# Performance work log

Hardware: AMD Instinct MI355X
Metric: run time of the kernel (lower is better)

The kernel has to match this reference:

```python
import jax, jax.numpy as jnp
import numpy as np

S, N, C = 256, 512, 32   # n_seq, n_res, channels
EPS = 1e-3               # module eps for mask normalization
LN_EPS = 1e-5            # torch LayerNorm default eps


def setup_inputs() -> dict:
    key = jax.random.key(0)
    ks = jax.random.split(key, 6)
    scale = 1.0 / np.sqrt(C)
    return {
        "m": jax.random.normal(ks[0], (S, N, C), jnp.float32),
        "mask": jnp.ones((S, N), jnp.float32),
        "ln_gamma": jnp.ones((C,), jnp.float32),
        "ln_beta": jnp.zeros((C,), jnp.float32),
        "Wa": jax.random.normal(ks[1], (C, C), jnp.float32) * scale,
        "ba": jnp.zeros((C,), jnp.float32),
        "Wb": jax.random.normal(ks[2], (C, C), jnp.float32) * scale,
        "bb": jnp.zeros((C,), jnp.float32),
        "Wout": jax.random.normal(ks[3], (C * C, C), jnp.float32) * (1.0 / np.sqrt(C * C)),
        "bout": jnp.zeros((C,), jnp.float32),
    }


def reference(m, mask, ln_gamma, ln_beta, Wa, ba, Wb, bb, Wout, bout):
    # LayerNorm over channel dim
    mu = jnp.mean(m, axis=-1, keepdims=True)
    var = jnp.mean(jnp.square(m - mu), axis=-1, keepdims=True)
    mh = (m - mu) * jax.lax.rsqrt(var + LN_EPS) * ln_gamma + ln_beta  # [S, N, C]

    # dual linear projections, masked per (seq, res), then seq<->res transpose
    a = jnp.swapaxes((mh @ Wa + ba) * mask[..., None], -2, -3)  # [N, S, C]
    b = jnp.swapaxes((mh @ Wb + bb) * mask[..., None], -2, -3)  # [N, S, C]

    # outer product summed over sequences: [N, N, C, C] -> [N, N, C*C]
    outer = jnp.einsum("bac,dae->bdce", a, b).reshape(N, N, C * C)
    outer = outer @ Wout + bout  # [N, N, C]

    # pairwise mask normalization: sum over seqs of mask[s,i]*mask[s,j]
    norm = jnp.einsum("ab,ad->bd", mask, mask)[..., None] + EPS  # [N, N, 1]
    return outer / norm
```

## Files before the change

### kernel.cpp

```cpp
#include <hip/hip_runtime.h>

#define S_SEQ 256
#define N_RES 512
#define CCH   32

typedef __attribute__((ext_vector_type(8))) short bf16x8;
typedef __attribute__((ext_vector_type(4))) float f32x4;
typedef __attribute__((ext_vector_type(2))) unsigned int u32x2;

__device__ __forceinline__ unsigned short f2bf(float x) {
    unsigned int u = __float_as_uint(x);
    return (unsigned short)((u + 0x7FFFu + ((u >> 16) & 1u)) >> 16);
}

#define GLOAD_LDS16(gp, lp) __builtin_amdgcn_global_load_lds( \
    (const __attribute__((address_space(1))) unsigned int*)(gp), \
    (__attribute__((address_space(3))) unsigned int*)(lp), 16, 0, 0)

#define BAR()    do { __builtin_amdgcn_s_barrier(); asm volatile("" ::: "memory"); } while (0)
#define WLGKM0() asm volatile("s_waitcnt lgkmcnt(0)" ::: "memory")
#define WVM(n)   asm volatile("s_waitcnt vmcnt(" #n ")" ::: "memory")

__global__ __launch_bounds__(256) void prep_ab(
    const float* __restrict__ m, const float* __restrict__ mask,
    const float* __restrict__ gam, const float* __restrict__ bet,
    const float* __restrict__ Wa, const float* __restrict__ ba,
    const float* __restrict__ Wb, const float* __restrict__ bb,
    char* __restrict__ Ag, char* __restrict__ Bg)
{
    __shared__ float WaL[1024], WbL[1024];
    __shared__ float gL[32], btL[32], baL[32], bbL[32];
    __shared__ unsigned short At[32 * 256];
    __shared__ unsigned short Bt[32 * 256];

    const int n = blockIdx.x;
    const int t = threadIdx.x;

    for (int i = t; i < 1024; i += 256) { WaL[i] = Wa[i]; WbL[i] = Wb[i]; }
    if (t < 32) { gL[t] = gam[t]; btL[t] = bet[t]; baL[t] = ba[t]; bbL[t] = bb[t]; }
    __syncthreads();

    const int s = t;
    float mv[32];
    const float* mrow = m + ((size_t)s * N_RES + n) * CCH;
#pragma unroll
    for (int c4 = 0; c4 < 8; c4++) {
        f32x4 v = *(const f32x4*)(mrow + c4 * 4);
        mv[c4 * 4 + 0] = v.x; mv[c4 * 4 + 1] = v.y;
        mv[c4 * 4 + 2] = v.z; mv[c4 * 4 + 3] = v.w;
    }
    float mu = 0.f;
#pragma unroll
    for (int c = 0; c < 32; c++) mu += mv[c];
    mu *= (1.f / 32.f);
    float var = 0.f;
#pragma unroll
    for (int c = 0; c < 32; c++) { float d = mv[c] - mu; var += d * d; }
    var *= (1.f / 32.f);
    float rs = rsqrtf(var + 1e-5f);
    float mh[32];
#pragma unroll
    for (int c = 0; c < 32; c++) mh[c] = (mv[c] - mu) * rs * gL[c] + btL[c];

    const float msk = mask[(size_t)s * N_RES + n];

    f32x4 av[8], bv[8];
#pragma unroll
    for (int cg = 0; cg < 8; cg++) { av[cg] = (f32x4)0.f; bv[cg] = (f32x4)0.f; }
#pragma unroll
    for (int k = 0; k < 32; k++) {
        float x = mh[k];
#pragma unroll
        for (int cg = 0; cg < 8; cg++) {
            f32x4 wa4 = *(const f32x4*)&WaL[k * 32 + cg * 4];
            f32x4 wb4 = *(const f32x4*)&WbL[k * 32 + cg * 4];
            av[cg] += x * wa4;
            bv[cg] += x * wb4;
        }
    }
#pragma unroll
    for (int cg = 0; cg < 8; cg++) {
#pragma unroll
        for (int u = 0; u < 4; u++) {
            int c = cg * 4 + u;
            At[c * 256 + s] = f2bf((av[cg][u] + baL[c]) * msk);
            Bt[c * 256 + s] = f2bf((bv[cg][u] + bbL[c]) * msk);
        }
    }
    __syncthreads();

    const size_t tbase = (size_t)(n >> 2) * 65536;
    const int halfq = ((n >> 1) & 1) << 2;
    const int irb = (n & 1) * 32;
#pragma unroll
    for (int u = 0; u < 4; u++) {
        int cid = t * 4 + u;
        int c = cid >> 5, g = cid & 31;
        int kt = g >> 2, q = g & 3;
        size_t off = tbase + (size_t)kt * 8192 + (size_t)(irb + c) * 128
                   + (size_t)(((halfq | q) ^ (c & 7)) << 4);
        *(uint4*)(Ag + off) = *(const uint4*)(At + c * 256 + g * 8);
        *(uint4*)(Bg + off) = *(const uint4*)(Bt + c * 256 + g * 8);
    }
}

__global__ __launch_bounds__(256) void kwt(const float* __restrict__ Wout,
                                           unsigned short* __restrict__ Wt3)
{
    int idx = blockIdx.x * 256 + threadIdx.x;
    int e = idx >> 10, ch = (idx >> 5) & 31, c = idx & 31;
    Wt3[idx] = f2bf(Wout[(size_t)(c * 32 + e) * 32 + ch]);
}

__global__ __launch_bounds__(256) void knorm(const float* __restrict__ mask,
                                             float* __restrict__ inv_norm)
{
    __shared__ float Mi[64][65];
    __shared__ float Mj[64][65];
    const int bi = blockIdx.x >> 3, bj = blockIdx.x & 7;
    const int t = threadIdx.x;
    const int ty = t >> 4, tx = t & 15;

    float acc[4][4];
#pragma unroll
    for (int a = 0; a < 4; a++)
#pragma unroll
        for (int b = 0; b < 4; b++) acc[a][b] = 0.f;

    for (int sc = 0; sc < 4; sc++) {
        for (int e = t; e < 4096; e += 256) {
            int sr = e >> 6, col = e & 63;
            Mi[sr][col] = mask[(size_t)(sc * 64 + sr) * N_RES + bi * 64 + col];
            Mj[sr][col] = mask[(size_t)(sc * 64 + sr) * N_RES + bj * 64 + col];
        }
        __syncthreads();
        for (int sp = 0; sp < 64; sp++) {
#pragma unroll
            for (int a = 0; a < 4; a++)
#pragma unroll
                for (int b = 0; b < 4; b++)
                    acc[a][b] += Mi[sp][ty * 4 + a] * Mj[sp][tx * 4 + b];
        }
        __syncthreads();
    }
#pragma unroll
    for (int a = 0; a < 4; a++)
#pragma unroll
        for (int b = 0; b < 4; b++) {
            int i = bi * 64 + ty * 4 + a;
            int j = bj * 64 + tx * 4 + b;
            inv_norm[(size_t)i * N_RES + j] = 1.f / (acc[a][b] + 1e-3f);
        }
}

__global__ __launch_bounds__(256, 4) void kmain9(
    const char* __restrict__ Ag, const char* __restrict__ Bg,
    const unsigned short* __restrict__ Wt3, const float* __restrict__ inv_norm,
    const float* __restrict__ bout, float* __restrict__ out)
{
    __shared__ __align__(16) char sm[33024];

    const int bid = blockIdx.x;
    const int xcd = bid & 7;
    const int xidx = bid >> 3;
    const int TI = xcd * 16 + ((xidx >> 5) & 15);
    const int TJ = (xidx >> 9) * 32 + (xidx & 31);

    const int t = threadIdx.x;
    const int lane = t & 63, wid = t >> 6;
    const int wr = wid >> 1, wc = wid & 1;
    const int rl = lane & 15, h4 = lane >> 4;

    const char* pa = Ag + (size_t)TI * 65536;
    const char* pb = Bg + (size_t)TJ * 65536;

#define SH(kt) do { \
    char* db_ = sm + (((kt) & 1) * 16384); \
    GLOAD_LDS16(pa + (kt) * 8192 + t * 16,        db_ + t * 16); \
    GLOAD_LDS16(pa + (kt) * 8192 + 4096 + t * 16, db_ + 4096 + t * 16); \
    GLOAD_LDS16(pb + (kt) * 8192 + t * 16,        db_ + 8192 + t * 16); \
    GLOAD_LDS16(pb + (kt) * 8192 + 4096 + t * 16, db_ + 12288 + t * 16); \
} while (0)

    const int abase = rl * 128 + (((((wr << 2) | h4)) ^ (rl & 7)) << 4);
    const int bbase = 8192 + rl * 128 + (((((wc << 2) | h4)) ^ (rl & 7)) << 4);

    f32x4 acc[4][4];
#pragma unroll
    for (int a = 0; a < 4; a++)
#pragma unroll
        for (int b = 0; b < 4; b++) acc[a][b] = (f32x4)0.f;

    SH(0);
    SH(1);

#pragma unroll
    for (int kt = 0; kt < 8; kt++) {
        if (kt < 7) { WVM(4); } else { WVM(0); }
        BAR();
        const char* buf = sm + ((kt & 1) * 16384);
        bf16x8 af[4], bfr[4];
#pragma unroll
        for (int am = 0; am < 4; am++)
            af[am] = *(const bf16x8*)(buf + abase + am * 2048);
#pragma unroll
        for (int bn = 0; bn < 4; bn++)
            bfr[bn] = *(const bf16x8*)(buf + bbase + bn * 2048);
        __builtin_amdgcn_s_setprio(1);
#pragma unroll
        for (int am = 0; am < 4; am++)
#pragma unroll
            for (int bn = 0; bn < 4; bn++)
                acc[am][bn] = __builtin_amdgcn_mfma_f32_16x16x32_bf16(
                    af[am], bfr[bn], acc[am][bn], 0, 0, 0);
        __builtin_amdgcn_s_setprio(0);
        BAR();
        if (kt <= 5) SH(kt + 2);
    }
#undef SH

#pragma unroll
    for (int am = 0; am < 4; am++) {
        const int cs = ((am & 1) << 1) + (h4 >> 1);
#pragma unroll
        for (int bn = 0; bn < 4; bn++) {
            const int p = (wr * 2 + (am >> 1)) * 4 + wc * 2 + (bn >> 1);
            const int e = ((bn & 1) << 4) + rl;
            unsigned int lo = (unsigned int)f2bf(acc[am][bn][0]) |
                              ((unsigned int)f2bf(acc[am][bn][1]) << 16);
            unsigned int hi = (unsigned int)f2bf(acc[am][bn][2]) |
                              ((unsigned int)f2bf(acc[am][bn][3]) << 16);
            u32x2 wv; wv[0] = lo; wv[1] = hi;
            *(u32x2*)(sm + p * 2064 + e * 64 +
                      ((cs ^ ((e >> 1) & 3)) << 4) + ((h4 & 1) << 3)) = wv;
        }
    }
    WLGKM0();
    BAR();

    const int kq = wid;
    f32x4 ae0 = (f32x4)0.f, ae1 = (f32x4)0.f;
    const char* grow = sm + rl * 2064;
#pragma unroll
    for (int es = 0; es < 8; es++) {
        const int e = kq * 8 + es;
        bf16x8 ga = *(const bf16x8*)(grow + e * 64 + ((h4 ^ ((e >> 1) & 3)) << 4));
        bf16x8 wb0 = *(const bf16x8*)(Wt3 + (size_t)e * 1024 + rl * 32 + h4 * 8);
        bf16x8 wb1 = *(const bf16x8*)(Wt3 + (size_t)e * 1024 + (16 + rl) * 32 + h4 * 8);
        ae0 = __builtin_amdgcn_mfma_f32_16x16x32_bf16(ga, wb0, ae0, 0, 0, 0);
        ae1 = __builtin_amdgcn_mfma_f32_16x16x32_bf16(ga, wb1, ae1, 0, 0, 0);
    }
    BAR();

    float* ps = (float*)sm;
#pragma unroll
    for (int r = 0; r < 4; r++) {
        ps[(kq * 16 + h4 * 4 + r) * 34 + rl]      = ae0[r];
        ps[(kq * 16 + h4 * 4 + r) * 34 + 16 + rl] = ae1[r];
    }
    WLGKM0();
    BAR();

#pragma unroll
    for (int u = 0; u < 2; u++) {
        const int idx = u * 256 + t;
        const int p = idx >> 5, ch = idx & 31;
        float v = 0.f;
#pragma unroll
        for (int k2 = 0; k2 < 4; k2++)
            v += ps[(k2 * 16 + p) * 34 + ch];
        const int i = TI * 4 + (p >> 2), j = TJ * 4 + (p & 3);
        out[((size_t)(i * N_RES + j)) * CCH + ch] =
            (v + bout[ch]) * inv_norm[(size_t)i * N_RES + j];
    }
}

extern "C" void kernel_launch(void* const* d_in, const int* in_sizes, int n_in,
                              void* d_out, int out_size, void* d_ws, size_t ws_size,
                              hipStream_t stream)
{
    const float* m    = (const float*)d_in[0];
    const float* mask = (const float*)d_in[1];
    const float* gam  = (const float*)d_in[2];
    const float* bet  = (const float*)d_in[3];
    const float* Wa   = (const float*)d_in[4];
    const float* ba   = (const float*)d_in[5];
    const float* Wb   = (const float*)d_in[6];
    const float* bb   = (const float*)d_in[7];
    const float* Wout = (const float*)d_in[8];
    const float* bout = (const float*)d_in[9];
    float* out = (float*)d_out;

    char* ws = (char*)d_ws;
    char* Ag = ws;
    char* Bg = ws + 8388608;
    unsigned short* Wt3 = (unsigned short*)(ws + 16777216);
    float* inv_norm = (float*)(ws + 16842752);

    prep_ab<<<dim3(N_RES), dim3(256), 0, stream>>>(m, mask, gam, bet, Wa, ba, Wb, bb, Ag, Bg);
    kwt<<<dim3(128), dim3(256), 0, stream>>>(Wout, Wt3);
    knorm<<<dim3(64), dim3(256), 0, stream>>>(mask, inv_norm);
    kmain9<<<dim3(16384), dim3(256), 0, stream>>>(Ag, Bg, Wt3, inv_norm, bout, out);
}
```

Baseline: 202.0 us.

## Load A operand directly from global into registers, stage only B in LDS

The prep kernel now writes A in a plain row-major layout, so the main kernel can load A fragments straight from global memory into registers, prefetching the next k-step after the MFMAs. Only B is staged through LDS, halving the LDS buffer traffic and shared-memory stage size. The bf16 packing of the accumulators also switches to the hardware v_cvt_pk_bf16_f32 instruction. The trade-off is that the direct global loads of A may expose latency, and rounding could differ slightly from the manual conversion.

After: 354.2 us. 75.4% more time.

```diff
diff --git a/kernel.cpp b/kernel.cpp
--- a/kernel.cpp
+++ b/kernel.cpp
@@ -11,6 +11,12 @@
 __device__ __forceinline__ unsigned short f2bf(float x) {
     unsigned int u = __float_as_uint(x);
     return (unsigned short)((u + 0x7FFFu + ((u >> 16) & 1u)) >> 16);
+}
+
+__device__ __forceinline__ unsigned int cvtpk(float lo, float hi) {
+    unsigned int r;
+    asm("v_cvt_pk_bf16_f32 %0, %1, %2" : "=v"(r) : "v"(lo), "v"(hi));
+    return r;
 }
 
 #define GLOAD_LDS16(gp, lp) __builtin_amdgcn_global_load_lds( \
@@ -89,7 +95,7 @@
     }
     __syncthreads();
 
-    const size_t tbase = (size_t)(n >> 2) * 65536;
+    const size_t tbB = (size_t)(n >> 2) * 65536;
     const int halfq = ((n >> 1) & 1) << 2;
     const int irb = (n & 1) * 32;
 #pragma unroll
@@ -97,10 +103,11 @@
         int cid = t * 4 + u;
         int c = cid >> 5, g = cid & 31;
         int kt = g >> 2, q = g & 3;
-        size_t off = tbase + (size_t)kt * 8192 + (size_t)(irb + c) * 128
-                   + (size_t)(((halfq | q) ^ (c & 7)) << 4);
-        *(uint4*)(Ag + off) = *(const uint4*)(At + c * 256 + g * 8);
-        *(uint4*)(Bg + off) = *(const uint4*)(Bt + c * 256 + g * 8);
+        size_t offA = (size_t)(n * 32 + c) * 512 + (size_t)g * 16;
+        size_t offB = tbB + (size_t)kt * 8192 + (size_t)(irb + c) * 128
+                    + (size_t)(((halfq | q) ^ (c & 7)) << 4);
+        *(uint4*)(Ag + offA) = *(const uint4*)(At + c * 256 + g * 8);
+        *(uint4*)(Bg + offB) = *(const uint4*)(Bt + c * 256 + g * 8);
     }
 }
 
@@ -153,7 +160,7 @@
         }
 }
 
-__global__ __launch_bounds__(256, 4) void kmain9(
+__global__ __launch_bounds__(256, 4) void kmain11(
     const char* __restrict__ Ag, const char* __restrict__ Bg,
     const unsigned short* __restrict__ Wt3, const float* __restrict__ inv_norm,
     const float* __restrict__ bout, float* __restrict__ out)
@@ -171,19 +178,17 @@
     const int wr = wid >> 1, wc = wid & 1;
     const int rl = lane & 15, h4 = lane >> 4;
 
-    const char* pa = Ag + (size_t)TI * 65536;
+    const char* pA = Ag + (size_t)TI * 65536;
     const char* pb = Bg + (size_t)TJ * 65536;
 
-#define SH(kt) do { \
-    char* db_ = sm + (((kt) & 1) * 16384); \
-    GLOAD_LDS16(pa + (kt) * 8192 + t * 16,        db_ + t * 16); \
-    GLOAD_LDS16(pa + (kt) * 8192 + 4096 + t * 16, db_ + 4096 + t * 16); \
-    GLOAD_LDS16(pb + (kt) * 8192 + t * 16,        db_ + 8192 + t * 16); \
-    GLOAD_LDS16(pb + (kt) * 8192 + 4096 + t * 16, db_ + 12288 + t * 16); \
+#define SB(kt) do { \
+    char* db_ = sm + (((kt) & 1) * 8192); \
+    GLOAD_LDS16(pb + (kt) * 8192 + t * 16,        db_ + t * 16); \
+    GLOAD_LDS16(pb + (kt) * 8192 + 4096 + t * 16, db_ + 4096 + t * 16); \
 } while (0)
 
-    const int abase = rl * 128 + (((((wr << 2) | h4)) ^ (rl & 7)) << 4);
-    const int bbase = 8192 + rl * 128 + (((((wc << 2) | h4)) ^ (rl & 7)) << 4);
+    const int abase = (wr * 64 + rl) * 512 + h4 * 16;
+    const int bbase = rl * 128 + ((((wc << 2) | h4) ^ (rl & 7)) << 4);
 
     f32x4 acc[4][4];
 #pragma unroll
@@ -191,18 +196,19 @@
 #pragma unroll
         for (int b = 0; b < 4; b++) acc[a][b] = (f32x4)0.f;
 
-    SH(0);
-    SH(1);
+    bf16x8 af[4];
+#pragma unroll
+    for (int am = 0; am < 4; am++)
+        af[am] = *(const bf16x8*)(pA + abase + am * 8192);
+    SB(0);
+    SB(1);
 
 #pragma unroll
     for (int kt = 0; kt < 8; kt++) {
-        if (kt < 7) { WVM(4); } else { WVM(0); }
+        if (kt < 7) { WVM(2); } else { WVM(0); }
         BAR();
-        const char* buf = sm + ((kt & 1) * 16384);
-        bf16x8 af[4], bfr[4];
-#pragma unroll
-        for (int am = 0; am < 4; am++)
-            af[am] = *(const bf16x8*)(buf + abase + am * 2048);
+        const char* buf = sm + ((kt & 1) * 8192);
+        bf16x8 bfr[4];
 #pragma unroll
         for (int bn = 0; bn < 4; bn++)
             bfr[bn] = *(const bf16x8*)(buf + bbase + bn * 2048);
@@ -214,10 +220,15 @@
                 acc[am][bn] = __builtin_amdgcn_mfma_f32_16x16x32_bf16(
                     af[am], bfr[bn], acc[am][bn], 0, 0, 0);
         __builtin_amdgcn_s_setprio(0);
+        if (kt < 7) {
+#pragma unroll
+            for (int am = 0; am < 4; am++)
+                af[am] = *(const bf16x8*)(pA + abase + am * 8192 + (kt + 1) * 64);
+        }
         BAR();
-        if (kt <= 5) SH(kt + 2);
-    }
-#undef SH
+        if (kt <= 5) SB(kt + 2);
+    }
+#undef SB
 
 #pragma unroll
     for (int am = 0; am < 4; am++) {
@@ -226,11 +237,9 @@
         for (int bn = 0; bn < 4; bn++) {
             const int p = (wr * 2 + (am >> 1)) * 4 + wc * 2 + (bn >> 1);
             const int e = ((bn & 1) << 4) + rl;
-            unsigned int lo = (unsigned int)f2bf(acc[am][bn][0]) |
-                              ((unsigned int)f2bf(acc[am][bn][1]) << 16);
-            unsigned int hi = (unsigned int)f2bf(acc[am][bn][2]) |
-                              ((unsigned int)f2bf(acc[am][bn][3]) << 16);
-            u32x2 wv; wv[0] = lo; wv[1] = hi;
+            u32x2 wv;
+            wv[0] = cvtpk(acc[am][bn][0], acc[am][bn][1]);
+            wv[1] = cvtpk(acc[am][bn][2], acc[am][bn][3]);
             *(u32x2*)(sm + p * 2064 + e * 64 +
                       ((cs ^ ((e >> 1) & 3)) << 4) + ((h4 & 1) << 3)) = wv;
         }
@@ -300,5 +309,5 @@
     prep_ab<<<dim3(N_RES), dim3(256), 0, stream>>>(m, mask, gam, bet, Wa, ba, Wb, bb, Ag, Bg);
     kwt<<<dim3(128), dim3(256), 0, stream>>>(Wout, Wt3);
     knorm<<<dim3(64), dim3(256), 0, stream>>>(mask, inv_norm);
-    kmain9<<<dim3(16384), dim3(256), 0, stream>>>(Ag, Bg, Wt3, inv_norm, bout, out);
-}
+    kmain11<<<dim3(16384), dim3(256), 0, stream>>>(Ag, Bg, Wt3, inv_norm, bout, out);
+}
```
